# Performance work log

Hardware: AMD Instinct MI355X
Metric: run time of the kernel (lower is better)

## Reference

```python
import jax, jax.numpy as jnp
import numpy as np

EPS = 1e-8


def conv3x3(x, w):
    # x: [B,C,H,W], w: [O,C,3,3], stride 1, pad 1, no bias
    return jax.lax.conv_general_dilated(x, w, (1, 1), [(1, 1), (1, 1)],
                                        dimension_numbers=("NCHW", "OIHW", "NCHW"))


def _bilinear_gather(x, py, px):
    # x: [B,C,H,W]; py,px: [B,K,H,W] float sample coordinates (y,x)
    B, C, H, W = x.shape
    y0 = jnp.floor(py)
    x0 = jnp.floor(px)
    wy1 = py - y0
    wx1 = px - x0
    wy0 = 1.0 - wy1
    wx0 = 1.0 - wx1

    def gather(yi, xi):
        valid = ((yi >= 0) & (yi < H) & (xi >= 0) & (xi < W)).astype(x.dtype)
        yc = jnp.clip(yi, 0, H - 1).astype(jnp.int32)
        xc = jnp.clip(xi, 0, W - 1).astype(jnp.int32)
        # per-batch advanced gather -> [B,C,K,H,W]
        g = jax.vmap(lambda xb, y_, x_: xb[:, y_, x_])(x, yc, xc)
        return g * valid[:, None]

    out = (gather(y0, x0) * (wy0 * wx0)[:, None]
           + gather(y0, x0 + 1) * (wy0 * wx1)[:, None]
           + gather(y0 + 1, x0) * (wy1 * wx0)[:, None]
           + gather(y0 + 1, x0 + 1) * (wy1 * wx1)[:, None])
    return out  # [B,C,K,H,W]


def deform_conv(x, offset, weight, pad):
    # ConvOffset2d (DCNv1, no modulation), stride 1, dilation 1, no bias.
    # offset: [B, 2*K, H, W], interleaved (dy, dx) per kernel point.
    B, C, H, W = x.shape
    O, Ci, kh, kw = weight.shape
    K = kh * kw
    off = offset.reshape(B, K, 2, H, W)
    dy, dx = off[:, :, 0], off[:, :, 1]                      # [B,K,H,W]
    ki, kj = jnp.meshgrid(jnp.arange(kh), jnp.arange(kw), indexing="ij")
    ki = ki.reshape(K).astype(x.dtype)
    kj = kj.reshape(K).astype(x.dtype)
    hh = jnp.arange(H, dtype=x.dtype)
    ww = jnp.arange(W, dtype=x.dtype)
    py = dy + ki[None, :, None, None] - pad + hh[None, None, :, None]
    px = dx + kj[None, :, None, None] - pad + ww[None, None, None, :]
    samp = _bilinear_gather(x, py, px)                        # [B,C,K,H,W]
    return jnp.einsum("bckhw,ock->bohw", samp, weight.reshape(O, Ci, K))


def _stsn_offset(x, y, off_ws, def_ws):
    feat = jnp.concatenate([x, y], axis=1)
    for i in range(3):
        off = conv3x3(feat, off_ws[i])
        feat = deform_conv(feat, off, def_ws[i], 1)
    return conv3x3(feat, off_ws[3])


def _S(x, s_ws):
    h = jax.nn.relu(conv3x3(x, s_ws[0]))
    h = jax.nn.relu(conv3x3(h, s_ws[1]))
    return jax.nn.relu(conv3x3(h, s_ws[2]))


def _cos_sim(a, b):
    # torch.F.cosine_similarity over channel dim (dim=1), eps=1e-8
    num = jnp.sum(a * b, axis=1)
    den = jnp.sqrt(jnp.maximum(jnp.sum(a * a, axis=1) * jnp.sum(b * b, axis=1), EPS * EPS))
    return num / den


def _forward(inputs, off_w0, off_w1, off_w2, off_w3, def_w0, def_w1, def_w2,
             pred_w, s_w1, s_w2, s_w3):
    off_ws = [off_w0, off_w1, off_w2, off_w3]
    def_ws = [def_w0, def_w1, def_w2]
    s_ws = [s_w1, s_w2, s_w3]
    x = inputs[0::2]
    y = inputs[1::2]
    offset0 = _stsn_offset(x, y, off_ws, def_ws)
    deform0 = deform_conv(x, offset0, pred_w, 1)
    weight0 = _S(deform0, s_ws)
    offset1 = _stsn_offset(y, y, off_ws, def_ws)
    deform1 = deform_conv(y, offset1, pred_w, 1)
    weight1 = _S(deform1, s_ws)
    Wx = _cos_sim(weight0, weight1)                           # [B,H,W]
    Wy = _cos_sim(weight1, weight1)
    wts = jax.nn.softmax(jnp.stack([Wx, Wy], axis=1), axis=1)  # [B,2,H,W]
    return deform0 * wts[:, 0:1] + deform1 * wts[:, 1:2]


def _conv_w(key, o, i, k=3):
    fan_in = i * k * k
    return jax.random.normal(key, (o, i, k, k), dtype=jnp.float32) / np.float32(np.sqrt(fan_in))


def setup_inputs() -> dict:
    key = jax.random.key(0)
    ks = jax.random.split(key, 16)
    IN_CH, OUT_CH, KS = 128, 128, 3
    C2 = 2 * IN_CH  # channels inside STSN_Offset
    inp = {
        "d1": jax.random.normal(ks[0], (1,), jnp.float32),
        "d2": jax.random.normal(ks[1], (1,), jnp.float32),
        "inputs": jax.random.normal(ks[2], (4, IN_CH, 64, 64), jnp.float32),
        "off_w0": _conv_w(ks[3], 2 * KS * KS, C2),
        "off_w1": _conv_w(ks[4], 2 * KS * KS, C2),
        "off_w2": _conv_w(ks[5], 2 * KS * KS, C2),
        "off_w3": _conv_w(ks[6], 2 * KS * KS, C2),
        "def_w0": _conv_w(ks[7], C2, C2),
        "def_w1": _conv_w(ks[8], C2, C2),
        "def_w2": _conv_w(ks[9], C2, C2),
        "pred_w": _conv_w(ks[10], OUT_CH, IN_CH),
        "s_w1": _conv_w(ks[11], OUT_CH // 2, OUT_CH),
        "s_w2": _conv_w(ks[12], OUT_CH // 4, OUT_CH // 2),
        "s_w3": _conv_w(ks[13], 1, OUT_CH // 4),
    }
    return inp


def reference(d1, d2, inputs, off_w0, off_w1, off_w2, off_w3, def_w0, def_w1,
              def_w2, pred_w, s_w1, s_w2, s_w3):
    # d1, d2 are accepted but unused, matching the torch module's forward.
    return _forward(inputs, off_w0, off_w1, off_w2, off_w3, def_w0, def_w1,
                    def_w2, pred_w, s_w1, s_w2, s_w3)
```

## Files before the change

kernel.cpp:

```cpp
#include <hip/hip_runtime.h>
#include <type_traits>

#define HD 64
#define WD 64
#define HW 4096
#define BATCH 2
#define NSLOT 4

typedef double v4d __attribute__((ext_vector_type(4)));
typedef double d2t __attribute__((ext_vector_type(2)));
typedef d2t d2u __attribute__((aligned(8)));
typedef float f2t __attribute__((ext_vector_type(2)));
typedef f2t f2u __attribute__((aligned(4)));

__global__ void pack_a_def_k(const float* __restrict__ w0, const float* __restrict__ w1,
                             const float* __restrict__ w2, float* __restrict__ pa) {
    int idx = blockIdx.x * 256 + threadIdx.x;
    if (idx >= 2 * 3 * 4 * 576 * 64 * 4) return;
    int tl = idx & 3;
    int l  = (idx >> 2) & 63;
    int m  = (idx >> 8) % 576;
    int rest = (idx >> 8) / 576;
    int wv = rest & 3;
    int Lc = rest >> 2;
    int conv = Lc % 3, L = Lc / 3;
    int a_i = L ? (l >> 2) : (l & 15);
    int a_k = L ? (l & 3)  : (l >> 4);
    int kk = 4 * m + a_k;
    int c = kk / 9, k = kk % 9;
    int o = wv * 64 + tl * 16 + a_i;
    const float* w = (conv == 0) ? w0 : (conv == 1) ? w1 : w2;
    pa[idx] = w[((size_t)o * 256 + c) * 9 + k];
}

__global__ void pack_a_pred_k(const float* __restrict__ w, float* __restrict__ pa) {
    int idx = blockIdx.x * 256 + threadIdx.x;
    if (idx >= 2 * 2 * 288 * 64 * 4) return;
    int tl = idx & 3;
    int l  = (idx >> 2) & 63;
    int m  = (idx >> 8) % 288;
    int rest = (idx >> 8) / 288;
    int wv = rest & 1, L = rest >> 1;
    int a_i = L ? (l >> 2) : (l & 15);
    int a_k = L ? (l & 3)  : (l >> 4);
    int kk = 4 * m + a_k;
    int c = kk / 9, k = kk % 9;
    int o = wv * 64 + tl * 16 + a_i;
    pa[idx] = w[((size_t)o * 128 + c) * 9 + k];
}

__global__ void transpose_ow4_k(const float* __restrict__ w0, const float* __restrict__ w1,
                                const float* __restrict__ w2, const float* __restrict__ w3,
                                float* __restrict__ owt) {
    const int N = 256 * 180;
    int idx = blockIdx.x * 256 + threadIdx.x;
    if (idx >= 4 * N) return;
    int which = idx / N, r = idx % N;
    const float* w = (which == 0) ? w0 : (which == 1) ? w1 : (which == 2) ? w2 : w3;
    int k20 = r % 20;
    int kk  = (r / 20) % 9;
    int c   = r / 180;
    owt[idx] = (k20 < 18) ? w[((size_t)k20 * 256 + c) * 9 + kk] : 0.f;
}

__global__ void pack_feat4_d(const float* __restrict__ in, double* __restrict__ dst) {
    int idx = blockIdx.x * 256 + threadIdx.x;
    if (idx >= NSLOT * 256 * HW) return;
    int i = idx % HW;
    int c = (idx / HW) & 255;
    int s = idx / (256 * HW);
    int b = s & 1, br = s >> 1;
    int img = (c < 128) ? (2 * b + br) : (2 * b + 1);
    dst[idx] = (double)in[((size_t)(img * 128 + (c & 127))) * HW + i];
}

__device__ __forceinline__ void probe_mfma_f64(
    int lane, int& aL1, int& b_k, int& b_j, int row_map[4], int col_map[4]) {
    v4d z = {0.0, 0.0, 0.0, 0.0};
    v4d pA = __builtin_amdgcn_mfma_f64_16x16x4f64((double)lane, 1.0, z, 0, 0, 0);
    v4d pB = __builtin_amdgcn_mfma_f64_16x16x4f64(1.0, (double)lane, z, 0, 0, 0);
    int vA = (int)pA[0];
    aL1 = ((vA & 3) != 0);
    int vB = (int)pB[0];
    if ((vB & 3) == 0) { b_j = lane & 15; b_k = lane >> 4; }
    else               { b_j = lane >> 2; b_k = lane & 3; }
#pragma unroll
    for (int r = 0; r < 4; ++r) {
        int va = (int)pA[r];
        row_map[r] = ((va & 3) == 0) ? (va - 96) >> 2 : (va - 6) >> 4;
        int vb = (int)pB[r];
        col_map[r] = ((vb & 3) == 0) ? (vb - 96) >> 2 : (vb - 6) >> 4;
    }
}

template <int O, int CC, bool PRED>
__global__ __launch_bounds__(O) void fused_deform_d(
    const double* __restrict__ csrc,
    const float*  __restrict__ owt,
    const float*  __restrict__ fsrc,
    const float4* __restrict__ pa,
    int paL1off,
    double* __restrict__ dst, int Ci) {
    constexpr int NCGT = O / 16;
    constexpr int CPG  = 256 / NCGT;
    constexpr int KC   = CC * 9;
    constexpr int NELEM = CC * 144;
    constexpr int NR   = NELEM / O;
    constexpr int REM  = NELEM % O;
    constexpr int NG   = CC;
    static_assert(2 * KC * 17 >= NG * 288, "phase-0 scratch");
    static_assert(NCGT % NG == 0, "phase-0 rounds");
    static_assert(KC % 4 == 0, "K steps");

    int px0 = blockIdx.x * 16;
    int h   = blockIdx.y;
    int s   = blockIdx.z;
    int t   = threadIdx.x;

    __shared__ double s_samp[2][KC * 17];
    __shared__ int    s_addr2[9][16][2];
    __shared__ double s_w4[9][16][4];
    __shared__ double s_off[18][16];

    {
        int px = t & 15, cg = t >> 4;
        int gx = px0 + px;
        double part[18];
#pragma unroll
        for (int k = 0; k < 18; ++k) part[k] = 0.0;
        const double* fb = csrc + (size_t)s * 256 * HW;
        bool ym = (h > 0), yp = (h < HD - 1), xm = (gx > 0), xp = (gx < WD - 1);
        for (int cc = 0; cc < CPG; ++cc) {
            int c = cg * CPG + cc;
            const double* fc = fb + (size_t)c * HW + h * WD + gx;
            double v[9];
            v[0] = (ym && xm) ? fc[-WD - 1] : 0.0;
            v[1] = ym ? fc[-WD] : 0.0;
            v[2] = (ym && xp) ? fc[-WD + 1] : 0.0;
            v[3] = xm ? fc[-1] : 0.0;
            v[4] = fc[0];
            v[5] = xp ? fc[1] : 0.0;
            v[6] = (yp && xm) ? fc[WD - 1] : 0.0;
            v[7] = yp ? fc[WD] : 0.0;
            v[8] = (yp && xp) ? fc[WD + 1] : 0.0;
            const float* wr = owt + (size_t)c * 180;
#pragma unroll
            for (int kk = 0; kk < 9; ++kk) {
                float wl[20];
                ((float4*)wl)[0] = *(const float4*)(wr + kk * 20);
                ((float4*)wl)[1] = *(const float4*)(wr + kk * 20 + 4);
                ((float4*)wl)[2] = *(const float4*)(wr + kk * 20 + 8);
                ((float4*)wl)[3] = *(const float4*)(wr + kk * 20 + 12);
                ((float4*)wl)[4] = *(const float4*)(wr + kk * 20 + 16);
                double vv = v[kk];
#pragma unroll
                for (int k = 0; k < 18; ++k)
                    part[k] = fma(vv, (double)wl[k], part[k]);
            }
        }
        double* s_part = &s_samp[0][0];
        for (int r0 = 0; r0 < NCGT; r0 += NG) {
            if (cg >= r0 && cg < r0 + NG) {
#pragma unroll
                for (int k = 0; k < 18; ++k)
                    s_part[((size_t)(cg - r0) * 18 + k) * 16 + px] = part[k];
            }
            __syncthreads();
            for (int i = t; i < 288; i += O) {
                int k = i >> 4, p2 = i & 15;
                double ssum = 0.0;
                for (int g = 0; g < NG; ++g)
                    ssum += s_part[((size_t)g * 18 + k) * 16 + p2];
                if (r0 == 0) s_off[k][p2] = ssum;
                else         s_off[k][p2] += ssum;
            }
            __syncthreads();
        }
    }

    for (int i = t; i < 144; i += O) {
        int k = i / 16, px = i % 16, wc = px0 + px;
        double dy = s_off[2 * k][px];
        double dx = s_off[2 * k + 1][px];
        double py  = dy + (double)(k / 3 - 1 + h);
        double pxf = dx + (double)(k % 3 - 1 + wc);
        double y0f = floor(py), x0f = floor(pxf);
        double wy1 = py - y0f, wx1 = pxf - x0f;
        double wy0 = 1.0 - wy1, wx0 = 1.0 - wx1;
        double y0c = fmax(-2.0, fmin(66.0, y0f));
        double x0c = fmax(-2.0, fmin(66.0, x0f));
        int y0 = (int)y0c, x0 = (int)x0c;
        int y1 = y0 + 1,   x1 = x0 + 1;
        bool vy0 = (y0 >= 0 && y0 < HD), vy1 = (y1 >= 0 && y1 < HD);
        bool vx0 = (x0 >= 0 && x0 < WD), vx1 = (x1 >= 0 && x1 < WD);
        int yc0 = min(max(y0, 0), HD - 1), yc1 = min(max(y1, 0), HD - 1);
        int xbase = min(max(x0, 0), WD - 2);
        s_addr2[k][px][0] = yc0 * WD + xbase;
        s_addr2[k][px][1] = yc1 * WD + xbase;
        bool sel0 = (x0 >= WD - 1);
        bool sel1 = (x0 >= 0);
        double wx0v = vx0 ? wx0 : 0.0;
        double wx1v = vx1 ? wx1 : 0.0;
        s_w4[k][px][0] = (sel0 ? 0.0 : wx0v) + (sel1 ? 0.0 : wx1v);
        s_w4[k][px][1] = (sel0 ? wx0v : 0.0) + (sel1 ? wx1v : 0.0);
        s_w4[k][px][2] = vy0 ? wy0 : 0.0;
        s_w4[k][px][3] = vy1 ? wy1 : 0.0;
    }
    __syncthreads();

    int b = s & 1, br = s >> 1;
    const double* srcb_d = csrc + (size_t)s * 256 * HW;
    const float*  srcb_f = PRED ? (fsrc + (size_t)(2 * b + br) * 128 * HW) : nullptr;

    using PairT = typename std::conditional<PRED, f2u, d2u>::type;
    PairT rp0[NR + 1], rp1[NR + 1];

    auto stage_issue = [&](int c0) {
#pragma unroll
        for (int n = 0; n <= NR; ++n) {
            if (n == NR && (REM == 0 || t >= REM)) continue;
            int i = t + n * O;
            int px = i & 15, kk = (i >> 4) % 9, c = i / 144;
            int a0 = s_addr2[kk][px][0], a1 = s_addr2[kk][px][1];
            if constexpr (PRED) {
                const float* p = srcb_f + (size_t)(c0 + c) * HW;
                rp0[n] = *(const f2u*)(p + a0);
                rp1[n] = *(const f2u*)(p + a1);
            } else {
                const double* p = srcb_d + (size_t)(c0 + c) * HW;
                rp0[n] = *(const d2u*)(p + a0);
                rp1[n] = *(const d2u*)(p + a1);
            }
        }
    };
    auto stage_finish = [&](int buf) {
#pragma unroll
        for (int n = 0; n <= NR; ++n) {
            if (n == NR && (REM == 0 || t >= REM)) continue;
            int i = t + n * O;
            int px = i & 15, kk = (i >> 4) % 9, c = i / 144;
            const double* wq = s_w4[kk][px];
            double r0 = (double)rp0[n].x * wq[0] + (double)rp0[n].y * wq[1];
            double r1 = (double)rp1[n].x * wq[0] + (double)rp1[n].y * wq[1];
            s_samp[buf][(c * 9 + kk) * 17 + px] = wq[2] * r0 + wq[3] * r1;
        }
    };

    int lane = t & 63;
    int wvid = t >> 6;
    int o0w  = wvid * 64;

    int aL1, b_k, b_j;
    int row_map[4], col_map[4];
    probe_mfma_f64(lane, aL1, b_k, b_j, row_map, col_map);

    size_t TOTM = (size_t)Ci * 9 / 4;
    const float4* wp0 = pa + (aL1 ? (size_t)paL1off : 0)
                      + (size_t)wvid * TOTM * 64 + lane;

    v4d acc[4];
#pragma unroll
    for (int tl = 0; tl < 4; ++tl) acc[tl] = (v4d){0.0, 0.0, 0.0, 0.0};

    stage_issue(0);
    stage_finish(0);
    __syncthreads();

    const int nch = Ci / CC;
    for (int ch = 0; ch < nch; ++ch) {
        int cur = ch & 1;
        bool more = (ch + 1 < nch);
        if (more) stage_issue((ch + 1) * CC);
        {
            const double* sb = &s_samp[cur][0];
            const float4* wp = wp0 + (size_t)ch * (KC / 4) * 64;
#pragma unroll
            for (int m = 0; m < KC / 4; ++m) {
                float4 av = wp[(size_t)m * 64];
                double bval = sb[(4 * m + b_k) * 17 + b_j];
                acc[0] = __builtin_amdgcn_mfma_f64_16x16x4f64((double)av.x, bval, acc[0], 0, 0, 0);
                acc[1] = __builtin_amdgcn_mfma_f64_16x16x4f64((double)av.y, bval, acc[1], 0, 0, 0);
                acc[2] = __builtin_amdgcn_mfma_f64_16x16x4f64((double)av.z, bval, acc[2], 0, 0, 0);
                acc[3] = __builtin_amdgcn_mfma_f64_16x16x4f64((double)av.w, bval, acc[3], 0, 0, 0);
            }
        }
        if (more) stage_finish(cur ^ 1);
        __syncthreads();
    }
#pragma unroll
    for (int tl = 0; tl < 4; ++tl) {
#pragma unroll
        for (int r = 0; r < 4; ++r) {
            int o = o0w + tl * 16 + row_map[r];
            dst[((size_t)(s * O + o) * HD + h) * WD + px0 + col_map[r]] = acc[tl][r];
        }
    }
}

__global__ __launch_bounds__(256) void conv3x3_s4_d(
    const double* __restrict__ src, const float* __restrict__ w,
    double* __restrict__ dst, int Ci, int O, int relu) {
    int idx = blockIdx.x * 256 + threadIdx.x;
    int px   = idx & 4095;
    int rest = idx >> 12;
    int og   = rest % (O >> 2);
    int img  = rest / (O >> 2);
    if (img >= NSLOT) return;
    int x = px & 63, h = px >> 6;
    const double* sb = src + (size_t)img * Ci * HW + h * WD + x;
    bool ym = (h > 0), yp = (h < HD - 1), xm = (x > 0), xp = (x < WD - 1);
    double acc[4] = {0.0, 0.0, 0.0, 0.0};
    for (int c = 0; c < Ci; ++c) {
        const double* sc = sb + (size_t)c * HW;
        double v[9];
        v[0] = (ym && xm) ? sc[-WD - 1] : 0.0;
        v[1] = ym ? sc[-WD] : 0.0;
        v[2] = (ym && xp) ? sc[-WD + 1] : 0.0;
        v[3] = xm ? sc[-1] : 0.0;
        v[4] = sc[0];
        v[5] = xp ? sc[1] : 0.0;
        v[6] = (yp && xm) ? sc[WD - 1] : 0.0;
        v[7] = yp ? sc[WD] : 0.0;
        v[8] = (yp && xp) ? sc[WD + 1] : 0.0;
#pragma unroll
        for (int oi = 0; oi < 4; ++oi) {
            const float* wc = w + ((size_t)(og * 4 + oi) * Ci + c) * 9;
#pragma unroll
            for (int k = 0; k < 9; ++k)
                acc[oi] = fma(v[k], (double)wc[k], acc[oi]);
        }
    }
#pragma unroll
    for (int oi = 0; oi < 4; ++oi) {
        double vv = acc[oi];
        if (relu) vv = fmax(vv, 0.0);
        dst[((size_t)(img * O + og * 4 + oi)) * HW + px] = vv;
    }
}

__global__ __launch_bounds__(256) void conv3x3_direct_d(
    const double* __restrict__ src, const float* __restrict__ w,
    double* __restrict__ dst, int Ci, int O, int relu) {
    int idx = blockIdx.x * 256 + threadIdx.x;
    int total = NSLOT * O * HW;
    if (idx >= total) return;
    int x = idx & (WD - 1);
    int h = (idx >> 6) & (HD - 1);
    int rest = idx >> 12;
    int o = rest % O;
    int img = rest / O;
    const double* s  = src + (size_t)img * Ci * HW + h * WD + x;
    const float*  wo = w + (size_t)o * Ci * 9;
    bool ym = (h > 0), yp = (h < HD - 1), xm = (x > 0), xp = (x < WD - 1);
    double a0 = 0.0, a1 = 0.0, a2 = 0.0;
    for (int c = 0; c < Ci; ++c) {
        const double* sc = s + (size_t)c * HW;
        const float*  wc = wo + c * 9;
        if (ym) {
            double v0 = xm ? sc[-WD - 1] : 0.0;
            double v1 = sc[-WD];
            double v2 = xp ? sc[-WD + 1] : 0.0;
            a0 = fma(v0, (double)wc[0], a0);
            a0 = fma(v1, (double)wc[1], a0);
            a0 = fma(v2, (double)wc[2], a0);
        }
        {
            double v0 = xm ? sc[-1] : 0.0;
            double v1 = sc[0];
            double v2 = xp ? sc[1] : 0.0;
            a1 = fma(v0, (double)wc[3], a1);
            a1 = fma(v1, (double)wc[4], a1);
            a1 = fma(v2, (double)wc[5], a1);
        }
        if (yp) {
            double v0 = xm ? sc[WD - 1] : 0.0;
            double v1 = sc[WD];
            double v2 = xp ? sc[WD + 1] : 0.0;
            a2 = fma(v0, (double)wc[6], a2);
            a2 = fma(v1, (double)wc[7], a2);
            a2 = fma(v2, (double)wc[8], a2);
        }
    }
    double acc = (a0 + a1) + a2;
    if (relu) acc = fmax(acc, 0.0);
    dst[idx] = acc;
}

__global__ void fuse_d(const double* __restrict__ dfm,
                       const double* __restrict__ wbuf,
                       float* __restrict__ out) {
    int idx = blockIdx.x * 256 + threadIdx.x;
    if (idx >= BATCH * 128 * HW) return;
    int i = idx % HW;
    int b = idx / (128 * HW);
    double a  = wbuf[(size_t)b * HW + i];
    double bb = wbuf[(size_t)(2 + b) * HW + i];
    double Wx = (a * bb) / sqrt(fmax((a * a) * (bb * bb), 1e-16));
    double Wy = (bb * bb) / sqrt(fmax((bb * bb) * (bb * bb), 1e-16));
    double m  = fmax(Wx, Wy);
    double e0 = exp(Wx - m), e1 = exp(Wy - m);
    double inv = 1.0 / (e0 + e1);
    double d0 = dfm[idx];
    double d1 = dfm[(size_t)2 * 128 * HW + idx];
    out[idx] = (float)((d0 * e0 + d1 * e1) * inv);
}

extern "C" void kernel_launch(void* const* d_in, const int* in_sizes, int n_in,
                              void* d_out, int out_size, void* d_ws, size_t ws_size,
                              hipStream_t stream) {
    const float* inputs = (const float*)d_in[2];
    const float* off_w[4] = {(const float*)d_in[3], (const float*)d_in[4],
                             (const float*)d_in[5], (const float*)d_in[6]};
    const float* def_w[3] = {(const float*)d_in[7], (const float*)d_in[8],
                             (const float*)d_in[9]};
    const float* pred_w = (const float*)d_in[10];
    const float* s_w[3] = {(const float*)d_in[11], (const float*)d_in[12],
                           (const float*)d_in[13]};
    float* out = (float*)d_out;

    double* ws = (double*)d_ws;
    size_t o = 0;
    double* featA = ws + o; o += (size_t)NSLOT * 256 * HW;
    double* featB = ws + o; o += (size_t)NSLOT * 256 * HW;
    float* owt    = (float*)(ws + o); o += (size_t)4 * 256 * 180 / 2;
    float* paDef  = (float*)(ws + o); o += (size_t)2 * 3 * 589824 / 2;
    float* paPred = (float*)(ws + o); o += (size_t)2 * 147456 / 2;
    if (ws_size < o * sizeof(double)) return;

    auto cdiv = [](int a, int b) { return (a + b - 1) / b; };

    pack_a_def_k<<<cdiv(2 * 3 * 589824, 256), 256, 0, stream>>>(
        def_w[0], def_w[1], def_w[2], paDef);
    pack_a_pred_k<<<cdiv(2 * 147456, 256), 256, 0, stream>>>(pred_w, paPred);
    transpose_ow4_k<<<cdiv(4 * 256 * 180, 256), 256, 0, stream>>>(
        off_w[0], off_w[1], off_w[2], off_w[3], owt);

    pack_feat4_d<<<cdiv(NSLOT * 256 * HW, 256), 256, 0, stream>>>(inputs, featB);

    dim3 dgrid(WD / 16, HD, NSLOT);
    const float4* paDef4  = (const float4*)paDef;
    const float4* paPred4 = (const float4*)paPred;
    const int PA_CONV = 589824 / 4;
    const int PA_L1_DEF = 3 * PA_CONV;
    const int PA_L1_PRED = 147456 / 4;

    double* cur = featB;
    double* nxt = featA;
    for (int i = 0; i < 3; ++i) {
        fused_deform_d<256, 8, false><<<dgrid, 256, 0, stream>>>(
            cur, owt + (size_t)i * 256 * 180, nullptr,
            paDef4 + (size_t)i * PA_CONV, PA_L1_DEF, nxt, 256);
        double* tmp = cur; cur = nxt; nxt = tmp;
    }
    double* deform = featB;
    double* s1     = featB + (size_t)NSLOT * 128 * HW;
    double* s2     = s1    + (size_t)NSLOT * 64 * HW;
    double* wbuf   = s2    + (size_t)NSLOT * 32 * HW;

    fused_deform_d<128, 4, true><<<dgrid, 128, 0, stream>>>(
        cur, owt + (size_t)3 * 256 * 180, inputs, paPred4, PA_L1_PRED, deform, 128);

    conv3x3_s4_d<<<cdiv(NSLOT * 16 * HW, 256), 256, 0, stream>>>(
        deform, s_w[0], s1, 128, 64, 1);
    conv3x3_s4_d<<<cdiv(NSLOT * 8 * HW, 256), 256, 0, stream>>>(
        s1, s_w[1], s2, 64, 32, 1);
    conv3x3_direct_d<<<cdiv(NSLOT * 1 * HW, 256), 256, 0, stream>>>(
        s2, s_w[2], wbuf, 32, 1, 1);

    fuse_d<<<cdiv(BATCH * 128 * HW, 256), 256, 0, stream>>>(deform, wbuf, out);
}
```

Measured before the change: 2.377 ms.

## Split deform conv input channels across two blocks with atomic accumulation

Doubles the grid of the fused deformable conv kernel so each block handles half of the input channels, and accumulates partial outputs into a zero-initialized destination with atomic adds. A zeroing kernel is launched before each deform layer. The launch bounds also request more resident blocks. This aims to raise occupancy and parallelism, but it recomputes the offset conv and bilinear weights in both halves, adds atomic traffic and zeroing passes, and makes summation order nondeterministic.

```diff
diff --git a/kernel.cpp b/kernel.cpp
--- a/kernel.cpp
+++ b/kernel.cpp
@@ -74,6 +74,11 @@
     dst[idx] = (double)in[((size_t)(img * 128 + (c & 127))) * HW + i];
 }
 
+__global__ void zero_d(double* __restrict__ p, int n) {
+    int i = blockIdx.x * 256 + threadIdx.x;
+    if (i < n) p[i] = 0.0;
+}
+
 __device__ __forceinline__ void probe_mfma_f64(
     int lane, int& aL1, int& b_k, int& b_j, int row_map[4], int col_map[4]) {
     v4d z = {0.0, 0.0, 0.0, 0.0};
@@ -94,7 +99,7 @@
 }
 
 template <int O, int CC, bool PRED>
-__global__ __launch_bounds__(O) void fused_deform_d(
+__global__ __launch_bounds__(O, 5) void fused_deform_d(
     const double* __restrict__ csrc,
     const float*  __restrict__ owt,
     const float*  __restrict__ fsrc,
@@ -114,7 +119,9 @@
 
     int px0 = blockIdx.x * 16;
     int h   = blockIdx.y;
-    int s   = blockIdx.z;
+    int zz  = blockIdx.z;
+    int s    = zz & (NSLOT - 1);
+    int half = zz >> 2;
     int t   = threadIdx.x;
 
     __shared__ double s_samp[2][KC * 17];
@@ -212,6 +219,9 @@
     const double* srcb_d = csrc + (size_t)s * 256 * HW;
     const float*  srcb_f = PRED ? (fsrc + (size_t)(2 * b + br) * 128 * HW) : nullptr;
 
+    const int chalf = Ci >> 1;
+    const int cbase = half * chalf;
+
     using PairT = typename std::conditional<PRED, f2u, d2u>::type;
     PairT rp0[NR + 1], rp1[NR + 1];
 
@@ -256,21 +266,22 @@
 
     size_t TOTM = (size_t)Ci * 9 / 4;
     const float4* wp0 = pa + (aL1 ? (size_t)paL1off : 0)
-                      + (size_t)wvid * TOTM * 64 + lane;
+                      + (size_t)wvid * TOTM * 64 + lane
+                      + (size_t)(half * (chalf * 9 / 4)) * 64;
 
     v4d acc[4];
 #pragma unroll
     for (int tl = 0; tl < 4; ++tl) acc[tl] = (v4d){0.0, 0.0, 0.0, 0.0};
 
-    stage_issue(0);
+    stage_issue(cbase);
     stage_finish(0);
     __syncthreads();
 
-    const int nch = Ci / CC;
+    const int nch = chalf / CC;
     for (int ch = 0; ch < nch; ++ch) {
         int cur = ch & 1;
         bool more = (ch + 1 < nch);
-        if (more) stage_issue((ch + 1) * CC);
+        if (more) stage_issue(cbase + (ch + 1) * CC);
         {
             const double* sb = &s_samp[cur][0];
             const float4* wp = wp0 + (size_t)ch * (KC / 4) * 64;
@@ -292,7 +303,8 @@
 #pragma unroll
         for (int r = 0; r < 4; ++r) {
             int o = o0w + tl * 16 + row_map[r];
-            dst[((size_t)(s * O + o) * HD + h) * WD + px0 + col_map[r]] = acc[tl][r];
+            unsafeAtomicAdd(&dst[((size_t)(s * O + o) * HD + h) * WD + px0 + col_map[r]],
+                            acc[tl][r]);
         }
     }
 }
@@ -437,16 +449,20 @@
 
     pack_feat4_d<<<cdiv(NSLOT * 256 * HW, 256), 256, 0, stream>>>(inputs, featB);
 
-    dim3 dgrid(WD / 16, HD, NSLOT);
+    dim3 dgrid(WD / 16, HD, NSLOT * 2);
     const float4* paDef4  = (const float4*)paDef;
     const float4* paPred4 = (const float4*)paPred;
     const int PA_CONV = 589824 / 4;
     const int PA_L1_DEF = 3 * PA_CONV;
     const int PA_L1_PRED = 147456 / 4;
 
+    const int NFEAT = NSLOT * 256 * HW;
+    const int NDEF  = NSLOT * 128 * HW;
+
     double* cur = featB;
     double* nxt = featA;
     for (int i = 0; i < 3; ++i) {
+        zero_d<<<cdiv(NFEAT, 256), 256, 0, stream>>>(nxt, NFEAT);
         fused_deform_d<256, 8, false><<<dgrid, 256, 0, stream>>>(
             cur, owt + (size_t)i * 256 * 180, nullptr,
             paDef4 + (size_t)i * PA_CONV, PA_L1_DEF, nxt, 256);
@@ -457,6 +473,7 @@
     double* s2     = s1    + (size_t)NSLOT * 64 * HW;
     double* wbuf   = s2    + (size_t)NSLOT * 32 * HW;
 
+    zero_d<<<cdiv(NDEF, 256), 256, 0, stream>>>(deform, NDEF);
     fused_deform_d<128, 4, true><<<dgrid, 128, 0, stream>>>(
         cur, owt + (size_t)3 * 256 * 180, inputs, paPred4, PA_L1_PRED, deform, 128);
 
```

After: 2.461 ms. 3.5% more time.

## Split fused deform kernel into producer waves (gather) and consumer waves (MFMA)

Applied to the files above, without the earlier changes.

Warp-specializes the fused deformable-conv kernel. Half the waves now only gather and bilinearly interpolate samples into a double-buffered shared tile, and the other half only run the f64 MFMA GEMM, each covering two 64-output tiles with eight accumulators. The goal is to overlap the irregular global gathers with the matrix work instead of having every wave alternate between them. In exchange, only half the waves issue MFMAs, each consumer wave holds twice the accumulator registers, and the barrier counts in the two paths must match exactly.

```diff
diff --git a/kernel.cpp b/kernel.cpp
--- a/kernel.cpp
+++ b/kernel.cpp
@@ -105,12 +105,16 @@
     constexpr int CPG  = 256 / NCGT;
     constexpr int KC   = CC * 9;
     constexpr int NELEM = CC * 144;
-    constexpr int NR   = NELEM / O;
-    constexpr int REM  = NELEM % O;
+    constexpr int NW   = O / 64;
+    constexpr int NCONS = NW / 2;
+    constexpr int PTH  = O / 2;
+    constexpr int NPR  = NELEM / PTH;
     constexpr int NG   = CC;
+    static_assert(NELEM % PTH == 0, "producer mapping");
     static_assert(2 * KC * 17 >= NG * 288, "phase-0 scratch");
     static_assert(NCGT % NG == 0, "phase-0 rounds");
     static_assert(KC % 4 == 0, "K steps");
+    static_assert(NW % 2 == 0, "wave split");
 
     int px0 = blockIdx.x * 16;
     int h   = blockIdx.y;
@@ -208,91 +212,102 @@
     }
     __syncthreads();
 
-    int b = s & 1, br = s >> 1;
-    const double* srcb_d = csrc + (size_t)s * 256 * HW;
-    const float*  srcb_f = PRED ? (fsrc + (size_t)(2 * b + br) * 128 * HW) : nullptr;
-
-    using PairT = typename std::conditional<PRED, f2u, d2u>::type;
-    PairT rp0[NR + 1], rp1[NR + 1];
-
-    auto stage_issue = [&](int c0) {
-#pragma unroll
-        for (int n = 0; n <= NR; ++n) {
-            if (n == NR && (REM == 0 || t >= REM)) continue;
-            int i = t + n * O;
-            int px = i & 15, kk = (i >> 4) % 9, c = i / 144;
-            int a0 = s_addr2[kk][px][0], a1 = s_addr2[kk][px][1];
-            if constexpr (PRED) {
-                const float* p = srcb_f + (size_t)(c0 + c) * HW;
-                rp0[n] = *(const f2u*)(p + a0);
-                rp1[n] = *(const f2u*)(p + a1);
-            } else {
-                const double* p = srcb_d + (size_t)(c0 + c) * HW;
-                rp0[n] = *(const d2u*)(p + a0);
-                rp1[n] = *(const d2u*)(p + a1);
-            }
-        }
-    };
-    auto stage_finish = [&](int buf) {
-#pragma unroll
-        for (int n = 0; n <= NR; ++n) {
-            if (n == NR && (REM == 0 || t >= REM)) continue;
-            int i = t + n * O;
-            int px = i & 15, kk = (i >> 4) % 9, c = i / 144;
-            const double* wq = s_w4[kk][px];
-            double r0 = (double)rp0[n].x * wq[0] + (double)rp0[n].y * wq[1];
-            double r1 = (double)rp1[n].x * wq[0] + (double)rp1[n].y * wq[1];
-            s_samp[buf][(c * 9 + kk) * 17 + px] = wq[2] * r0 + wq[3] * r1;
-        }
-    };
-
     int lane = t & 63;
     int wvid = t >> 6;
-    int o0w  = wvid * 64;
-
-    int aL1, b_k, b_j;
-    int row_map[4], col_map[4];
-    probe_mfma_f64(lane, aL1, b_k, b_j, row_map, col_map);
-
-    size_t TOTM = (size_t)Ci * 9 / 4;
-    const float4* wp0 = pa + (aL1 ? (size_t)paL1off : 0)
-                      + (size_t)wvid * TOTM * 64 + lane;
-
-    v4d acc[4];
-#pragma unroll
-    for (int tl = 0; tl < 4; ++tl) acc[tl] = (v4d){0.0, 0.0, 0.0, 0.0};
-
-    stage_issue(0);
-    stage_finish(0);
-    __syncthreads();
-
     const int nch = Ci / CC;
-    for (int ch = 0; ch < nch; ++ch) {
-        int cur = ch & 1;
-        bool more = (ch + 1 < nch);
-        if (more) stage_issue((ch + 1) * CC);
-        {
-            const double* sb = &s_samp[cur][0];
-            const float4* wp = wp0 + (size_t)ch * (KC / 4) * 64;
+
+    if (wvid >= NCONS) {
+        int b = s & 1, br = s >> 1;
+        const double* srcb_d = csrc + (size_t)s * 256 * HW;
+        const float*  srcb_f = PRED ? (fsrc + (size_t)(2 * b + br) * 128 * HW) : nullptr;
+        int pt = t - NCONS * 64;
+
+        using PairT = typename std::conditional<PRED, f2u, d2u>::type;
+        PairT rp0[NPR], rp1[NPR];
+
+        auto stage_issue = [&](int c0) {
+#pragma unroll
+            for (int n = 0; n < NPR; ++n) {
+                int i = pt + n * PTH;
+                int px = i & 15, kk = (i >> 4) % 9, c = i / 144;
+                int a0 = s_addr2[kk][px][0], a1 = s_addr2[kk][px][1];
+                if constexpr (PRED) {
+                    const float* p = srcb_f + (size_t)(c0 + c) * HW;
+                    rp0[n] = *(const f2u*)(p + a0);
+                    rp1[n] = *(const f2u*)(p + a1);
+                } else {
+                    const double* p = srcb_d + (size_t)(c0 + c) * HW;
+                    rp0[n] = *(const d2u*)(p + a0);
+                    rp1[n] = *(const d2u*)(p + a1);
+                }
+            }
+        };
+        auto stage_finish = [&](int buf) {
+#pragma unroll
+            for (int n = 0; n < NPR; ++n) {
+                int i = pt + n * PTH;
+                int px = i & 15, kk = (i >> 4) % 9, c = i / 144;
+                const double* wq = s_w4[kk][px];
+                double r0 = (double)rp0[n].x * wq[0] + (double)rp0[n].y * wq[1];
+                double r1 = (double)rp1[n].x * wq[0] + (double)rp1[n].y * wq[1];
+                s_samp[buf][(c * 9 + kk) * 17 + px] = wq[2] * r0 + wq[3] * r1;
+            }
+        };
+
+        stage_issue(0);
+        stage_finish(0);
+        __syncthreads();
+        for (int ch = 0; ch < nch; ++ch) {
+            if (ch + 1 < nch) {
+                stage_issue((ch + 1) * CC);
+                stage_finish((ch & 1) ^ 1);
+            }
+            __syncthreads();
+        }
+    } else {
+        int aL1, b_k, b_j;
+        int row_map[4], col_map[4];
+        probe_mfma_f64(lane, aL1, b_k, b_j, row_map, col_map);
+
+        size_t TOTM = (size_t)Ci * 9 / 4;
+        const float4* wpA = pa + (aL1 ? (size_t)paL1off : 0)
+                          + (size_t)(2 * wvid) * TOTM * 64 + lane;
+        const float4* wpB = wpA + TOTM * 64;
+
+        v4d acc[8];
+#pragma unroll
+        for (int tt = 0; tt < 8; ++tt) acc[tt] = (v4d){0.0, 0.0, 0.0, 0.0};
+
+        __syncthreads();
+        for (int ch = 0; ch < nch; ++ch) {
+            const double* sb = &s_samp[ch & 1][0];
+            const float4* pA = wpA + (size_t)ch * (KC / 4) * 64;
+            const float4* pB = wpB + (size_t)ch * (KC / 4) * 64;
 #pragma unroll
             for (int m = 0; m < KC / 4; ++m) {
-                float4 av = wp[(size_t)m * 64];
                 double bval = sb[(4 * m + b_k) * 17 + b_j];
-                acc[0] = __builtin_amdgcn_mfma_f64_16x16x4f64((double)av.x, bval, acc[0], 0, 0, 0);
-                acc[1] = __builtin_amdgcn_mfma_f64_16x16x4f64((double)av.y, bval, acc[1], 0, 0, 0);
-                acc[2] = __builtin_amdgcn_mfma_f64_16x16x4f64((double)av.z, bval, acc[2], 0, 0, 0);
-                acc[3] = __builtin_amdgcn_mfma_f64_16x16x4f64((double)av.w, bval, acc[3], 0, 0, 0);
-            }
-        }
-        if (more) stage_finish(cur ^ 1);
-        __syncthreads();
-    }
-#pragma unroll
-    for (int tl = 0; tl < 4; ++tl) {
-#pragma unroll
-        for (int r = 0; r < 4; ++r) {
-            int o = o0w + tl * 16 + row_map[r];
-            dst[((size_t)(s * O + o) * HD + h) * WD + px0 + col_map[r]] = acc[tl][r];
+                float4 a0 = pA[(size_t)m * 64];
+                float4 a1 = pB[(size_t)m * 64];
+                acc[0] = __builtin_amdgcn_mfma_f64_16x16x4f64((double)a0.x, bval, acc[0], 0, 0, 0);
+                acc[1] = __builtin_amdgcn_mfma_f64_16x16x4f64((double)a0.y, bval, acc[1], 0, 0, 0);
+                acc[2] = __builtin_amdgcn_mfma_f64_16x16x4f64((double)a0.z, bval, acc[2], 0, 0, 0);
+                acc[3] = __builtin_amdgcn_mfma_f64_16x16x4f64((double)a0.w, bval, acc[3], 0, 0, 0);
+                acc[4] = __builtin_amdgcn_mfma_f64_16x16x4f64((double)a1.x, bval, acc[4], 0, 0, 0);
+                acc[5] = __builtin_amdgcn_mfma_f64_16x16x4f64((double)a1.y, bval, acc[5], 0, 0, 0);
+                acc[6] = __builtin_amdgcn_mfma_f64_16x16x4f64((double)a1.z, bval, acc[6], 0, 0, 0);
+                acc[7] = __builtin_amdgcn_mfma_f64_16x16x4f64((double)a1.w, bval, acc[7], 0, 0, 0);
+            }
+            __syncthreads();
+        }
+#pragma unroll
+        for (int tt = 0; tt < 8; ++tt) {
+            int wv_eff = 2 * wvid + (tt >> 2);
+            int tl = tt & 3;
+#pragma unroll
+            for (int r = 0; r < 4; ++r) {
+                int o = wv_eff * 64 + tl * 16 + row_map[r];
+                dst[((size_t)(s * O + o) * HD + h) * WD + px0 + col_map[r]] = acc[tt][r];
+            }
         }
     }
 }
```

Result: slower. 2.957 ms (+24.4%).
